# Kernel tuning notes

Measured on AMD Instinct MI355X. Metric: run time of the kernel, lower is better.

## Reference

```python
import jax, jax.numpy as jnp
import numpy as np

N_NODES = 100000
N_EDGES = 1600000
NODE_DIM = 16
EDGE_DIM = 16
OUT_DIM = 16
H = 64  # edge/node/global hidden size
N_GRAPHS = 1


def _glorot(key, shape):
    fan_in, fan_out = shape[0], shape[1]
    lim = np.sqrt(6.0 / (fan_in + fan_out))
    return jax.random.uniform(key, shape, jnp.float32, -lim, lim)


def setup_inputs() -> dict:
    key = jax.random.key(0)
    ks = jax.random.split(key, 16)
    x = jax.random.normal(ks[0], (N_NODES, NODE_DIM), jnp.float32)
    edge_attr = jax.random.normal(ks[1], (N_EDGES, EDGE_DIM), jnp.float32)
    u = jax.random.normal(ks[2], (N_GRAPHS, H), jnp.float32)
    senders = jax.random.randint(ks[3], (N_EDGES,), 0, N_NODES, jnp.int32)
    receivers = jax.random.randint(ks[4], (N_EDGES,), 0, N_NODES, jnp.int32)
    node_gidx = jnp.zeros((N_NODES,), jnp.int32)
    edge_gidx = jnp.zeros((N_EDGES,), jnp.int32)
    # EdgeBlock MLP: in = edge + 2*node + global_h
    W_eb = _glorot(ks[5], (EDGE_DIM + 2 * NODE_DIM + H, H)); b_eb = jnp.zeros((H,), jnp.float32)
    # NodeBlock MLP: in = node + edge_h + global_h
    W_nb = _glorot(ks[6], (NODE_DIM + H + H, H)); b_nb = jnp.zeros((H,), jnp.float32)
    # GlobalBlock MLP: in = node_h + edge_h + global_h
    W_gb = _glorot(ks[7], (H + H + H, H)); b_gb = jnp.zeros((H,), jnp.float32)
    # node decoder: in = 2*edge_h + node_h + global_h -> H -> out
    W_d1 = _glorot(ks[8], (2 * H + H + H, H)); b_d1 = jnp.zeros((H,), jnp.float32)
    W_d2 = _glorot(ks[9], (H, OUT_DIM)); b_d2 = jnp.zeros((OUT_DIM,), jnp.float32)
    return dict(x=x, edge_attr=edge_attr, u=u, senders=senders, receivers=receivers,
                node_gidx=node_gidx, edge_gidx=edge_gidx,
                W_eb=W_eb, b_eb=b_eb, W_nb=W_nb, b_nb=b_nb, W_gb=W_gb, b_gb=b_gb,
                W_d1=W_d1, b_d1=b_d1, W_d2=W_d2, b_d2=b_d2)


def _segment_mean(data, ids, num_segments):
    s = jax.ops.segment_sum(data, ids, num_segments=num_segments)
    cnt = jax.ops.segment_sum(jnp.ones((data.shape[0], 1), data.dtype), ids, num_segments=num_segments)
    return s / jnp.maximum(cnt, 1.0)


def reference(x, edge_attr, u, senders, receivers, node_gidx, edge_gidx,
              W_eb, b_eb, W_nb, b_nb, W_gb, b_gb, W_d1, b_d1, W_d2, b_d2):
    # ---- GN1: EdgeBlock (gather -> concat -> linear+relu) ----
    e_in = jnp.concatenate([edge_attr, x[receivers], x[senders], u[edge_gidx]], axis=-1)  # [E, 112]
    e_h = jax.nn.relu(e_in @ W_eb + b_eb)  # [E, H]
    # ---- GN1: NodeBlock (scatter_add of received edges) ----
    agg_recv = jax.ops.segment_sum(e_h, receivers, num_segments=x.shape[0])  # [N, H]
    n_in = jnp.concatenate([agg_recv, x, u[node_gidx]], axis=-1)
    n_h = jax.nn.relu(n_in @ W_nb + b_nb)  # [N, H]
    # ---- GN1: GlobalBlock (scatter_mean reductions) ----
    e_mean = _segment_mean(e_h, edge_gidx, u.shape[0])  # [B, H]
    n_mean = _segment_mean(n_h, node_gidx, u.shape[0])  # [B, H]
    g_in = jnp.concatenate([e_mean, n_mean, u], axis=-1)
    u2 = jax.nn.relu(g_in @ W_gb + b_gb)  # [B, H]
    # ---- GN2: node decoder block (scatter_mean sent + received edges) ----
    agg_recv2 = _segment_mean(e_h, receivers, x.shape[0])
    agg_sent2 = _segment_mean(e_h, senders, x.shape[0])
    d_in = jnp.concatenate([agg_recv2, agg_sent2, n_h, u2[node_gidx]], axis=-1)  # [N, 256]
    out = jax.nn.relu(d_in @ W_d1 + b_d1) @ W_d2 + b_d2  # [N, out_dim]
    return out
```

## Files before the change

kernel.cpp:

```cpp
#include <hip/hip_runtime.h>


typedef unsigned int uint;
typedef unsigned short ushort;
typedef __attribute__((ext_vector_type(8))) short bf16x8;
typedef __attribute__((ext_vector_type(4))) float f32x4;

#define BW 128
#define BSHIFT 7
#define NBMAX 784
#define DC 4096
#define EMASK 0x1FFFFFu
#define OMASK 0x1FFFFu

#define LDF4(p) (*reinterpret_cast<const float4*>(p))

__device__ __forceinline__ ushort f2bf(float f) {
  uint u = __float_as_uint(f);
  u += 0x7FFFu + ((u >> 16) & 1u);
  return (ushort)(u >> 16);
}

__device__ __forceinline__ int aswz(int row, int kb) {
  return row * 64 + ((kb ^ (row & 7)) << 3);
}
__device__ __forceinline__ int nswz(int row, int kb) {
  return row * 128 + (((kb & 8) | ((kb ^ row) & 7)) << 3);
}
__device__ __forceinline__ int aswz192(int row, int kb) {
  return row * 192 + (((kb & 24) | ((kb ^ row) & 7)) << 3);
}

__global__ __launch_bounds__(256) void init_kernel(
    const float* __restrict__ x, ushort* __restrict__ xb, int n16,
    const float* __restrict__ u, const float* __restrict__ W_eb,
    const float* __restrict__ b_eb, const float* __restrict__ W_nb,
    const float* __restrict__ b_nb, const float* __restrict__ W_d1,
    const float* __restrict__ W_d2, float* __restrict__ eb_init,
    float* __restrict__ nb_init, ushort* __restrict__ wt_lin,
    ushort* __restrict__ wnb_img, ushort* __restrict__ wtd1_img,
    ushort* __restrict__ w2_img) {
  if (blockIdx.x == 0) {
    int j = threadIdx.x;
    if (j >= 64) return;
    float ae = b_eb[j], an = b_nb[j];
    for (int k = 0; k < 64; ++k) {
      float uk = u[k];
      ae = fmaf(uk, W_eb[(48 + k) * 64 + j], ae);
      an = fmaf(uk, W_nb[(80 + k) * 64 + j], an);
    }
    eb_init[j] = ae;
    nb_init[j] = an;
    for (int k = 0; k < 64; ++k)
      wt_lin[j * 64 + k] = (k < 48) ? f2bf(W_eb[k * 64 + j]) : (ushort)0;
    for (int k = 0; k < 128; ++k) {
      ushort v = (k < 80) ? f2bf(W_nb[k * 64 + j]) : (ushort)0;
      wnb_img[nswz(j, k >> 3) + (k & 7)] = v;
    }
    for (int k = 0; k < 192; ++k)
      wtd1_img[aswz192(j, k >> 3) + (k & 7)] = f2bf(W_d1[k * 64 + j]);
    if (j < 16)
      for (int k = 0; k < 64; ++k)
        w2_img[aswz(j, k >> 3) + (k & 7)] = f2bf(W_d2[k * 16 + j]);
    return;
  }
  int i = (blockIdx.x - 1) * 256 + threadIdx.x;
  if (i * 4 >= n16) return;
  float4 a = LDF4(x + i * 4);
  ushort4 o = {f2bf(a.x), f2bf(a.y), f2bf(a.z), f2bf(a.w)};
  *reinterpret_cast<ushort4*>(xb + i * 4) = o;
}

__global__ __launch_bounds__(256) void bcount_kernel(
    const int* __restrict__ receivers, const int* __restrict__ senders,
    uint* __restrict__ bcnt_r, uint* __restrict__ bcnt_s, int E, int NB) {
  __shared__ uint hr[NBMAX], hs[NBMAX];
  int t = threadIdx.x;
  for (int i = t; i < NB; i += 256) { hr[i] = 0; hs[i] = 0; }
  __syncthreads();
  int stride = gridDim.x * 256;
  for (int e = blockIdx.x * 256 + t; e < E; e += stride) {
    atomicAdd(&hr[receivers[e] >> BSHIFT], 1u);
    atomicAdd(&hs[senders[e] >> BSHIFT], 1u);
  }
  __syncthreads();
  for (int i = t; i < NB; i += 256) {
    if (hr[i]) atomicAdd(&bcnt_r[i], hr[i]);
    if (hs[i]) atomicAdd(&bcnt_s[i], hs[i]);
  }
}

__global__ __launch_bounds__(256) void bscan_kernel(
    const uint* __restrict__ bcnt_r, const uint* __restrict__ bcnt_s,
    uint* __restrict__ start_r, uint* __restrict__ start_s,
    uint* __restrict__ cur_r, uint* __restrict__ cur_s, int E, int NB) {
  __shared__ uint ts[256];
  int t = threadIdx.x;
  #pragma unroll
  for (int pass = 0; pass < 2; ++pass) {
    const uint* cnt = pass ? bcnt_s : bcnt_r;
    uint* start = pass ? start_s : start_r;
    uint* cur = pass ? cur_s : cur_r;
    uint loc[4]; uint tsum = 0;
    #pragma unroll
    for (int q = 0; q < 4; ++q) {
      int i = t * 4 + q;
      loc[q] = (i < NB) ? cnt[i] : 0;
      tsum += loc[q];
    }
    ts[t] = tsum;
    __syncthreads();
    for (int off = 1; off < 256; off <<= 1) {
      uint a = (t >= off) ? ts[t - off] : 0;
      __syncthreads();
      ts[t] += a;
      __syncthreads();
    }
    uint run = ts[t] - tsum;
    #pragma unroll
    for (int q = 0; q < 4; ++q) {
      int i = t * 4 + q;
      if (i < NB) { start[i] = run; cur[i] = run; run += loc[q]; }
    }
    if (t == 0) start[NB] = (uint)E;
    __syncthreads();
  }
}

__global__ __launch_bounds__(256) void distribute_kernel(
    const int* __restrict__ receivers, const int* __restrict__ senders,
    uint* __restrict__ gcur_r, uint* __restrict__ gcur_s,
    uint2* __restrict__ tmp_r, uint2* __restrict__ tmp_s, int E, int NB) {
  __shared__ uint hist[NBMAX], lstart[NBMAX], cur[NBMAX], gbase[NBMAX];
  __shared__ uint2 ids[DC];
  __shared__ ushort idsB[DC];
  __shared__ uint ts[256];
  int dir = blockIdx.x & 1;
  const int* key = dir ? senders : receivers;
  const int* oth = dir ? receivers : senders;
  uint* g_cursor = dir ? gcur_s : gcur_r;
  uint2* tmp = dir ? tmp_s : tmp_r;
  int t = threadIdx.x;
  int base = (blockIdx.x >> 1) * DC;
  int cact = min(DC, E - base);
  for (int i = t; i < NB; i += 256) hist[i] = 0;
  __syncthreads();
  for (int k = 0; k < DC / 256; ++k) {
    int j = k * 256 + t;
    if (j < cact) atomicAdd(&hist[key[base + j] >> BSHIFT], 1u);
  }
  __syncthreads();
  {
    uint loc[4]; uint tsum = 0;
    #pragma unroll
    for (int q = 0; q < 4; ++q) {
      int i = t * 4 + q;
      loc[q] = (i < NB) ? hist[i] : 0;
      tsum += loc[q];
    }
    ts[t] = tsum;
    __syncthreads();
    for (int off = 1; off < 256; off <<= 1) {
      uint a = (t >= off) ? ts[t - off] : 0;
      __syncthreads();
      ts[t] += a;
      __syncthreads();
    }
    uint run = ts[t] - tsum;
    #pragma unroll
    for (int q = 0; q < 4; ++q) {
      int i = t * 4 + q;
      if (i < NB) { lstart[i] = run; cur[i] = run; run += loc[q]; }
    }
  }
  __syncthreads();
  for (int i = t; i < NB; i += 256)
    if (hist[i]) gbase[i] = atomicAdd(&g_cursor[i], hist[i]);
  for (int k = 0; k < DC / 256; ++k) {
    int j = k * 256 + t;
    if (j < cact) {
      int e = base + j;
      int kk = key[e];
      uint b = (uint)(kk >> BSHIFT);
      uint slot = atomicAdd(&cur[b], 1u);
      ids[slot] = uint2{((uint)(kk & (BW - 1)) << 21) | (uint)e,
                        (uint)oth[e]};
      idsB[slot] = (ushort)b;
    }
  }
  __syncthreads();
  for (int j = t; j < cact; j += 256) {
    uint b2 = idsB[j];
    tmp[gbase[b2] + ((uint)j - lstart[b2])] = ids[j];
  }
}

__global__ __launch_bounds__(256) void bucketsort_kernel(
    const uint2* __restrict__ tmp_r, const uint2* __restrict__ tmp_s,
    const uint* __restrict__ start_r, const uint* __restrict__ start_s,
    uint2* __restrict__ srt_r, uint2* __restrict__ srt_s,
    uint* __restrict__ cnt_r, uint* __restrict__ cnt_s, int N) {
  __shared__ uint hist[BW], pfx[BW], cur[BW];
  int d = blockIdx.x & 1;
  int b = blockIdx.x >> 1;
  const uint2* tmp = d ? tmp_s : tmp_r;
  const uint* start = d ? start_s : start_r;
  uint2* srt = d ? srt_s : srt_r;
  uint* cnt = d ? cnt_s : cnt_r;
  int t = threadIdx.x;
  if (t < BW) hist[t] = 0;
  __syncthreads();
  int beg = (int)start[b], end = (int)start[b + 1];
  for (int i = beg + t; i < end; i += 256)
    atomicAdd(&hist[tmp[i].x >> 21], 1u);
  __syncthreads();
  if (t < BW) pfx[t] = hist[t];
  __syncthreads();
  for (int off = 1; off < BW; off <<= 1) {
    uint a = 0;
    if (t < BW && t >= off) a = pfx[t - off];
    __syncthreads();
    if (t < BW) pfx[t] += a;
    __syncthreads();
  }
  if (t < BW) cur[t] = pfx[t] - hist[t];
  __syncthreads();
  uint bhi = (uint)b << 17;
  for (int i = beg + t; i < end; i += 256) {
    uint2 v = tmp[i];
    uint nl = v.x >> 21;
    uint p = beg + atomicAdd(&cur[nl], 1u);
    srt[p] = uint2{v.x, bhi | v.y};
  }
  int nbase = b * BW;
  if (t < BW && nbase + t < N) cnt[nbase + t] = hist[t];
}

__global__ __launch_bounds__(256, 4) void escatter_kernel(
    const float* __restrict__ edge_attr, const ushort* __restrict__ xb,
    const uint2* __restrict__ srt_r, const uint2* __restrict__ srt_s,
    const ushort* __restrict__ wt_lin, const float* __restrict__ eb_init,
    float* __restrict__ sum_recv, float* __restrict__ sum_sent, int E,
    int ntiles) {
  __shared__ float Clds[4][16 * 72];
  __shared__ int nodeW[4][16];
  int t = threadIdx.x;
  int wid = t >> 6, l = t & 63;
  int lrow = l & 15, lk = l >> 4;
  bf16x8 b0[4], b1[4];
  float ebi[4];
  #pragma unroll
  for (int nt = 0; nt < 4; ++nt) {
    const ushort* wr = wt_lin + (nt * 16 + lrow) * 64;
    b0[nt] = *reinterpret_cast<const bf16x8*>(wr + lk * 8);
    b1[nt] = *reinterpret_cast<const bf16x8*>(wr + 32 + lk * 8);
    ebi[nt] = eb_init[nt * 16 + lrow];
  }
  const bf16x8 zero8 = {0, 0, 0, 0, 0, 0, 0, 0};
  int dir = blockIdx.x & 1;
  const uint2* srt = dir ? srt_s : srt_r;
  float* sum = dir ? sum_sent : sum_recv;
  int gw = (blockIdx.x >> 1) * 4 + wid;
  int nw = (gridDim.x >> 1) * 4;

  uint2 vC = {0, 0}, vN = {0, 0};
  bf16x8 a0C = zero8, a1C = zero8;

  if (gw < ntiles) {
    vC = srt[min(gw * 16 + lrow, E - 1)];
    int e = (int)(vC.x & EMASK);
    int kn = (int)((vC.y >> 17) * BW + (vC.x >> 21));
    int on = (int)(vC.y & OMASK);
    int s = dir ? kn : on;
    int r = dir ? on : kn;
    if (lk < 2) {
      const float* ap = edge_attr + (size_t)e * 16 + lk * 8;
      float4 f0 = LDF4(ap), f1 = LDF4(ap + 4);
      union { ushort h[8]; bf16x8 v; } pk;
      pk.h[0] = f2bf(f0.x); pk.h[1] = f2bf(f0.y);
      pk.h[2] = f2bf(f0.z); pk.h[3] = f2bf(f0.w);
      pk.h[4] = f2bf(f1.x); pk.h[5] = f2bf(f1.y);
      pk.h[6] = f2bf(f1.z); pk.h[7] = f2bf(f1.w);
      a0C = pk.v;
      a1C = *reinterpret_cast<const bf16x8*>(xb + (size_t)s * 16 + lk * 8);
    } else {
      a0C = *reinterpret_cast<const bf16x8*>(xb + (size_t)r * 16 +
                                             (lk - 2) * 8);
      a1C = zero8;
    }
  }
  if (gw + nw < ntiles) vN = srt[min((gw + nw) * 16 + lrow, E - 1)];

  for (int tile = gw; tile < ntiles; tile += nw) {
    bool hasN = (tile + nw) < ntiles;
    bool has2 = (tile + 2 * nw) < ntiles;
    bf16x8 a0N = zero8, a1N = zero8;
    if (hasN) {
      int e = (int)(vN.x & EMASK);
      int kn = (int)((vN.y >> 17) * BW + (vN.x >> 21));
      int on = (int)(vN.y & OMASK);
      int s = dir ? kn : on;
      int r = dir ? on : kn;
      if (lk < 2) {
        const float* ap = edge_attr + (size_t)e * 16 + lk * 8;
        float4 f0 = LDF4(ap), f1 = LDF4(ap + 4);
        union { ushort h[8]; bf16x8 v; } pk;
        pk.h[0] = f2bf(f0.x); pk.h[1] = f2bf(f0.y);
        pk.h[2] = f2bf(f0.z); pk.h[3] = f2bf(f0.w);
        pk.h[4] = f2bf(f1.x); pk.h[5] = f2bf(f1.y);
        pk.h[6] = f2bf(f1.z); pk.h[7] = f2bf(f1.w);
        a0N = pk.v;
        a1N = *reinterpret_cast<const bf16x8*>(xb + (size_t)s * 16 + lk * 8);
      } else {
        a0N = *reinterpret_cast<const bf16x8*>(xb + (size_t)r * 16 +
                                               (lk - 2) * 8);
      }
    }
    uint2 v2 = {0, 0};
    if (has2) v2 = srt[min((tile + 2 * nw) * 16 + lrow, E - 1)];
    if (lk == 0)
      nodeW[wid][lrow] = (int)((vC.y >> 17) * BW + (vC.x >> 21));
    f32x4 acc[4];
    #pragma unroll
    for (int nt = 0; nt < 4; ++nt) {
      acc[nt] = f32x4{ebi[nt], ebi[nt], ebi[nt], ebi[nt]};
      acc[nt] =
          __builtin_amdgcn_mfma_f32_16x16x32_bf16(a0C, b0[nt], acc[nt], 0, 0, 0);
      acc[nt] =
          __builtin_amdgcn_mfma_f32_16x16x32_bf16(a1C, b1[nt], acc[nt], 0, 0, 0);
    }
    int m0 = (l >> 4) * 4;
    #pragma unroll
    for (int nt = 0; nt < 4; ++nt) {
      #pragma unroll
      for (int reg = 0; reg < 4; ++reg) {
        Clds[wid][(m0 + reg) * 72 + nt * 16 + lrow] =
            fmaxf(acc[nt][reg], 0.f);
      }
    }
    int vc = min(16, E - tile * 16);
    float accum = 0.f;
    int prev = nodeW[wid][0];
    for (int mm = 0; mm < vc; ++mm) {
      int nd = nodeW[wid][mm];
      float v = Clds[wid][mm * 72 + l];
      if (nd != prev) {
        atomicAdd(&sum[(size_t)prev * 64 + l], accum);
        accum = 0.f;
        prev = nd;
      }
      accum += v;
    }
    atomicAdd(&sum[(size_t)prev * 64 + l], accum);
    vC = vN; a0C = a0N; a1C = a1N; vN = v2;
  }
}

__global__ __launch_bounds__(256, 2) void node_mfma_kernel(
    const float* __restrict__ sum_recv, const ushort* __restrict__ xb,
    const ushort* __restrict__ wnb_img, const float* __restrict__ nb_init,
    ushort* __restrict__ n_h, int N) {
  __shared__ ushort Alds[64 * 128];
  __shared__ ushort Wlds[64 * 128];
  __shared__ ushort Clds[4][16 * 72];
  int t = threadIdx.x;
  int base = blockIdx.x * 64;
  {
    const uint4* src = reinterpret_cast<const uint4*>(wnb_img);
    uint4* dst = reinterpret_cast<uint4*>(Wlds);
    #pragma unroll
    for (int i = 0; i < 4; ++i) dst[t + 256 * i] = src[t + 256 * i];
  }
  {
    int m = t >> 2, part = t & 3;
    int n = base + m;
    bool val = n < N;
    if (part < 2) {
      #pragma unroll
      for (int q = 0; q < 4; ++q) {
        int c = part * 4 + q;
        union { ushort h[8]; uint4 qq; } pk;
        if (val) {
          const float* src = sum_recv + (size_t)n * 64 + c * 8;
          float4 f0 = LDF4(src), f1 = LDF4(src + 4);
          pk.h[0] = f2bf(f0.x); pk.h[1] = f2bf(f0.y);
          pk.h[2] = f2bf(f0.z); pk.h[3] = f2bf(f0.w);
          pk.h[4] = f2bf(f1.x); pk.h[5] = f2bf(f1.y);
          pk.h[6] = f2bf(f1.z); pk.h[7] = f2bf(f1.w);
        } else {
          pk.qq = uint4{0, 0, 0, 0};
        }
        *reinterpret_cast<uint4*>(&Alds[nswz(m, c)]) = pk.qq;
      }
    } else if (part == 2) {
      uint4 w0 = {0, 0, 0, 0}, w1 = {0, 0, 0, 0};
      if (val) {
        const uint4* xp = reinterpret_cast<const uint4*>(xb + (size_t)n * 16);
        w0 = xp[0]; w1 = xp[1];
      }
      *reinterpret_cast<uint4*>(&Alds[nswz(m, 8)]) = w0;
      *reinterpret_cast<uint4*>(&Alds[nswz(m, 9)]) = w1;
      *reinterpret_cast<uint4*>(&Alds[nswz(m, 10)]) = uint4{0, 0, 0, 0};
      *reinterpret_cast<uint4*>(&Alds[nswz(m, 11)]) = uint4{0, 0, 0, 0};
    } else {
      #pragma unroll
      for (int q = 0; q < 4; ++q)
        *reinterpret_cast<uint4*>(&Alds[nswz(m, 12 + q)]) = uint4{0, 0, 0, 0};
    }
  }
  __syncthreads();
  int wid = t >> 6, l = t & 63;
  int lrow = l & 15, lk = l >> 4;
  int arow = wid * 16 + lrow;
  bf16x8 afr[4];
  #pragma unroll
  for (int g = 0; g < 4; ++g)
    afr[g] = *reinterpret_cast<const bf16x8*>(&Alds[nswz(arow, g * 4 + lk)]);
  f32x4 acc[4];
  #pragma unroll
  for (int nt = 0; nt < 4; ++nt) {
    float nbi = nb_init[nt * 16 + lrow];
    acc[nt] = f32x4{nbi, nbi, nbi, nbi};
    #pragma unroll
    for (int g = 0; g < 4; ++g) {
      bf16x8 b = *reinterpret_cast<const bf16x8*>(
          &Wlds[nswz(nt * 16 + lrow, g * 4 + lk)]);
      acc[nt] =
          __builtin_amdgcn_mfma_f32_16x16x32_bf16(afr[g], b, acc[nt], 0, 0, 0);
    }
  }
  int m0 = (l >> 4) * 4;
  #pragma unroll
  for (int nt = 0; nt < 4; ++nt) {
    #pragma unroll
    for (int reg = 0; reg < 4; ++reg) {
      Clds[wid][(m0 + reg) * 72 + nt * 16 + lrow] =
          f2bf(fmaxf(acc[nt][reg], 0.f));
    }
  }
  __syncthreads();
  int sm = l >> 2, ch = l & 3;
  int gn = base + wid * 16 + sm;
  uint4 c0 = *reinterpret_cast<const uint4*>(&Clds[wid][sm * 72 + ch * 16]);
  uint4 c1 = *reinterpret_cast<const uint4*>(&Clds[wid][sm * 72 + ch * 16 + 8]);
  if (gn < N) {
    uint4* dst = reinterpret_cast<uint4*>(n_h + (size_t)gn * 64 + ch * 16);
    dst[0] = c0;
    dst[1] = c1;
  }
}

__global__ __launch_bounds__(256) void reduce_kernel(
    const float* __restrict__ sum_recv, const ushort* __restrict__ n_h,
    float* __restrict__ e_sum, float* __restrict__ n_sum, int N) {
  __shared__ float ls[128];
  if (threadIdx.x < 128) ls[threadIdx.x] = 0.f;
  __syncthreads();
  int g = threadIdx.x & 15;
  int tid = blockIdx.x * blockDim.x + threadIdx.x;
  int row0 = tid >> 4;
  int rstride = (gridDim.x * blockDim.x) >> 4;
  float pe[4] = {0, 0, 0, 0}, pn[4] = {0, 0, 0, 0};
  for (int r = row0; r < N; r += rstride) {
    float4 a = LDF4(sum_recv + (size_t)r * 64 + g * 4);
    uint2 b = *reinterpret_cast<const uint2*>(n_h + (size_t)r * 64 + g * 4);
    pe[0] += a.x; pe[1] += a.y; pe[2] += a.z; pe[3] += a.w;
    pn[0] += __uint_as_float(b.x << 16);
    pn[1] += __uint_as_float(b.x & 0xFFFF0000u);
    pn[2] += __uint_as_float(b.y << 16);
    pn[3] += __uint_as_float(b.y & 0xFFFF0000u);
  }
  #pragma unroll
  for (int i = 0; i < 4; ++i) {
    atomicAdd(&ls[g * 4 + i], pe[i]);
    atomicAdd(&ls[64 + g * 4 + i], pn[i]);
  }
  __syncthreads();
  if (threadIdx.x < 64) {
    atomicAdd(&e_sum[threadIdx.x], ls[threadIdx.x]);
    atomicAdd(&n_sum[threadIdx.x], ls[64 + threadIdx.x]);
  }
}

__global__ void global_kernel(const float* __restrict__ u,
                              const float* __restrict__ e_sum,
                              const float* __restrict__ n_sum,
                              const float* __restrict__ W_gb,
                              const float* __restrict__ b_gb,
                              const float* __restrict__ W_d1,
                              const float* __restrict__ b_d1,
                              float* __restrict__ d1_init, float Ef, float Nf) {
  __shared__ float gin[192];
  __shared__ float u2s[64];
  int j = threadIdx.x;
  gin[j] = e_sum[j] / Ef;
  gin[64 + j] = n_sum[j] / Nf;
  gin[128 + j] = u[j];
  __syncthreads();
  float a = b_gb[j];
  for (int k = 0; k < 192; ++k) a = fmaf(gin[k], W_gb[k * 64 + j], a);
  u2s[j] = fmaxf(a, 0.f);
  __syncthreads();
  float d = b_d1[j];
  for (int k = 0; k < 64; ++k) d = fmaf(u2s[k], W_d1[(192 + k) * 64 + j], d);
  d1_init[j] = d;
}

__global__ __launch_bounds__(256, 2) void decoder_mfma_kernel(
    const float* __restrict__ sum_recv, const float* __restrict__ sum_sent,
    const uint* __restrict__ cnt_r, const uint* __restrict__ cnt_s,
    const ushort* __restrict__ n_h, const ushort* __restrict__ wtd1_img,
    const float* __restrict__ d1_init, const ushort* __restrict__ w2_img,
    const float* __restrict__ b_d2, float* __restrict__ out, int N) {
  __shared__ ushort Alds[64 * 192];
  __shared__ ushort Wlds[64 * 192];
  __shared__ ushort Hlds[64 * 64];
  __shared__ ushort W2lds[16 * 64];
  int t = threadIdx.x;
  int base = blockIdx.x * 64;
  {
    const uint4* src = reinterpret_cast<const uint4*>(wtd1_img);
    uint4* dst = reinterpret_cast<uint4*>(Wlds);
    #pragma unroll
    for (int i = 0; i < 6; ++i) dst[t + 256 * i] = src[t + 256 * i];
    if (t < 128)
      reinterpret_cast<uint4*>(W2lds)[t] =
          reinterpret_cast<const uint4*>(w2_img)[t];
  }
  {
    int m = t >> 2;
    int n = base + m;
    bool val = n < N;
    float invr = 0.f, invs = 0.f;
    if (val) {
      invr = 1.f / fmaxf((float)cnt_r[n], 1.f);
      invs = 1.f / fmaxf((float)cnt_s[n], 1.f);
    }
    int c0 = (t & 3) * 6;
    for (int c = c0; c < c0 + 6; ++c) {
      union { ushort h[8]; uint4 q; } pk;
      if (val) {
        if (c >= 16) {
          pk.q = *reinterpret_cast<const uint4*>(n_h + (size_t)n * 64 +
                                                 (c - 16) * 8);
        } else {
          const float* src;
          float scl;
          if (c < 8) { src = sum_recv + (size_t)n * 64 + c * 8; scl = invr; }
          else       { src = sum_sent + (size_t)n * 64 + (c - 8) * 8; scl = invs; }
          float4 f0 = LDF4(src), f1 = LDF4(src + 4);
          pk.h[0] = f2bf(f0.x * scl); pk.h[1] = f2bf(f0.y * scl);
          pk.h[2] = f2bf(f0.z * scl); pk.h[3] = f2bf(f0.w * scl);
          pk.h[4] = f2bf(f1.x * scl); pk.h[5] = f2bf(f1.y * scl);
          pk.h[6] = f2bf(f1.z * scl); pk.h[7] = f2bf(f1.w * scl);
        }
      } else {
        pk.q = uint4{0, 0, 0, 0};
      }
      *reinterpret_cast<uint4*>(&Alds[aswz192(m, c)]) = pk.q;
    }
  }
  __syncthreads();
  int wid = t >> 6, l = t & 63;
  int lrow = l & 15, lk = l >> 4;
  int arow = wid * 16 + lrow;
  bf16x8 afr[6];
  #pragma unroll
  for (int g = 0; g < 6; ++g)
    afr[g] = *reinterpret_cast<const bf16x8*>(&Alds[aswz192(arow, g * 4 + lk)]);
  f32x4 acc[4];
  #pragma unroll
  for (int nt = 0; nt < 4; ++nt) {
    float di = d1_init[nt * 16 + lrow];
    acc[nt] = f32x4{di, di, di, di};
    #pragma unroll
    for (int g = 0; g < 6; ++g) {
      bf16x8 b = *reinterpret_cast<const bf16x8*>(
          &Wlds[aswz192(nt * 16 + lrow, g * 4 + lk)]);
      acc[nt] =
          __builtin_amdgcn_mfma_f32_16x16x32_bf16(afr[g], b, acc[nt], 0, 0, 0);
    }
  }
  int m0 = (l >> 4) * 4;
  #pragma unroll
  for (int nt = 0; nt < 4; ++nt) {
    #pragma unroll
    for (int reg = 0; reg < 4; ++reg) {
      int hm = wid * 16 + m0 + reg;
      int hn = nt * 16 + lrow;
      Hlds[hm * 64 + (((hn >> 3) ^ (hm & 7)) << 3) + (hn & 7)] =
          f2bf(fmaxf(acc[nt][reg], 0.f));
    }
  }
  __syncthreads();
  bf16x8 a20 = *reinterpret_cast<const bf16x8*>(&Hlds[aswz(arow, lk)]);
  bf16x8 a21 = *reinterpret_cast<const bf16x8*>(&Hlds[aswz(arow, 4 + lk)]);
  bf16x8 b20 = *reinterpret_cast<const bf16x8*>(&W2lds[aswz(lrow, lk)]);
  bf16x8 b21 = *reinterpret_cast<const bf16x8*>(&W2lds[aswz(lrow, 4 + lk)]);
  float bi = b_d2[lrow];
  f32x4 o = f32x4{bi, bi, bi, bi};
  o = __builtin_amdgcn_mfma_f32_16x16x32_bf16(a20, b20, o, 0, 0, 0);
  o = __builtin_amdgcn_mfma_f32_16x16x32_bf16(a21, b21, o, 0, 0, 0);
  #pragma unroll
  for (int reg = 0; reg < 4; ++reg) {
    int ge = base + wid * 16 + m0 + reg;
    if (ge < N) out[(size_t)ge * 16 + lrow] = o[reg];
  }
}

extern "C" void kernel_launch(void* const* d_in, const int* in_sizes, int n_in,
                              void* d_out, int out_size, void* d_ws,
                              size_t ws_size, hipStream_t stream) {
  const float* x         = (const float*)d_in[0];
  const float* edge_attr = (const float*)d_in[1];
  const float* u         = (const float*)d_in[2];
  const int*   senders   = (const int*)d_in[3];
  const int*   receivers = (const int*)d_in[4];
  const float* W_eb = (const float*)d_in[7];
  const float* b_eb = (const float*)d_in[8];
  const float* W_nb = (const float*)d_in[9];
  const float* b_nb = (const float*)d_in[10];
  const float* W_gb = (const float*)d_in[11];
  const float* b_gb = (const float*)d_in[12];
  const float* W_d1 = (const float*)d_in[13];
  const float* b_d1 = (const float*)d_in[14];
  const float* W_d2 = (const float*)d_in[15];
  const float* b_d2 = (const float*)d_in[16];

  int N = in_sizes[0] / 16;
  int E = in_sizes[1] / 16;
  int NB = (N + BW - 1) >> BSHIFT;
  int NDB = (E + DC - 1) / DC;
  int ntiles = (E + 15) / 16;

  char* w = (char*)d_ws;
  float* sum_recv = (float*)w;       w += (size_t)N * 64 * 4;
  float* sum_sent = (float*)w;       w += (size_t)N * 64 * 4;
  ushort* n_h = (ushort*)w;          w += (size_t)N * 64 * 2;
  uint2* tmp_r = (uint2*)w;          w += (size_t)E * 8;
  uint2* tmp_s = (uint2*)w;          w += (size_t)E * 8;
  uint2* srt_r = (uint2*)w;          w += (size_t)E * 8;
  uint2* srt_s = (uint2*)w;          w += (size_t)E * 8;
  uint* cnt_r = (uint*)w;            w += (size_t)N * 4;
  uint* cnt_s = (uint*)w;            w += (size_t)N * 4;
  ushort* xb = (ushort*)w;           w += (size_t)N * 16 * 2;
  ushort* wt_lin = (ushort*)w;       w += (size_t)64 * 64 * 2;
  ushort* wnb_img = (ushort*)w;      w += (size_t)64 * 128 * 2;
  ushort* wtd1_img = (ushort*)w;     w += (size_t)64 * 192 * 2;
  ushort* w2_img = (ushort*)w;       w += (size_t)16 * 64 * 2;
  uint* start_r = (uint*)w;          w += (size_t)(NB + 1) * 4;
  uint* start_s = (uint*)w;          w += (size_t)(NB + 1) * 4;
  uint* cur_r = (uint*)w;            w += (size_t)NB * 4;
  uint* cur_s = (uint*)w;            w += (size_t)NB * 4;
  uint* bcnt_r = (uint*)w;           w += (size_t)NBMAX * 4;
  uint* bcnt_s = (uint*)w;           w += (size_t)NBMAX * 4;
  float* e_sum = (float*)w;          w += 64 * 4;
  float* n_sum = (float*)w;          w += 64 * 4;
  float* eb_init = (float*)w;        w += 64 * 4;
  float* nb_init = (float*)w;        w += 64 * 4;
  float* d1_init = (float*)w;        w += 64 * 4;

  size_t zero_bytes = (size_t)(2 * NBMAX + 128) * 4;
  hipMemsetAsync(bcnt_r, 0, zero_bytes, stream);
  hipMemsetAsync(sum_recv, 0, (size_t)N * 128 * 4, stream);

  hipLaunchKernelGGL(init_kernel, dim3(1 + (N * 16 / 4 + 255) / 256), dim3(256),
                     0, stream, x, xb, N * 16, u, W_eb, b_eb, W_nb, b_nb, W_d1,
                     W_d2, eb_init, nb_init, wt_lin, wnb_img, wtd1_img, w2_img);
  hipLaunchKernelGGL(bcount_kernel, dim3(64), dim3(256), 0, stream, receivers,
                     senders, bcnt_r, bcnt_s, E, NB);
  hipLaunchKernelGGL(bscan_kernel, dim3(1), dim3(256), 0, stream, bcnt_r,
                     bcnt_s, start_r, start_s, cur_r, cur_s, E, NB);
  hipLaunchKernelGGL(distribute_kernel, dim3(2 * NDB), dim3(256), 0, stream,
                     receivers, senders, cur_r, cur_s, tmp_r, tmp_s, E, NB);
  hipLaunchKernelGGL(bucketsort_kernel, dim3(2 * NB), dim3(256), 0, stream,
                     tmp_r, tmp_s, start_r, start_s, srt_r, srt_s, cnt_r,
                     cnt_s, N);
  hipLaunchKernelGGL(escatter_kernel, dim3(4096), dim3(256), 0, stream,
                     edge_attr, xb, srt_r, srt_s, wt_lin, eb_init, sum_recv,
                     sum_sent, E, ntiles);
  hipLaunchKernelGGL(node_mfma_kernel, dim3((N + 63) / 64), dim3(256), 0,
                     stream, sum_recv, xb, wnb_img, nb_init, n_h, N);
  hipLaunchKernelGGL(reduce_kernel, dim3(256), dim3(256), 0, stream, sum_recv,
                     n_h, e_sum, n_sum, N);
  hipLaunchKernelGGL(global_kernel, dim3(1), dim3(64), 0, stream, u, e_sum,
                     n_sum, W_gb, b_gb, W_d1, b_d1, d1_init, (float)E,
                     (float)N);
  hipLaunchKernelGGL(decoder_mfma_kernel, dim3((N + 63) / 64), dim3(256), 0,
                     stream, sum_recv, sum_sent, cnt_r, cnt_s, n_h, wtd1_img,
                     d1_init, w2_img, b_d2, (float*)d_out, N);
}
```

Before: 416.2 us.

## Fuse bucket count into init, global reductions into node kernel, global MLP into decoder

Merges the bucket-count kernel into the init kernel as extra blocks, folds the edge and node mean reductions into node_mfma_kernel's epilogue, and recomputes the global MLP (u2 and d1_init) redundantly in every decoder block. The escatter segmented reduction now precomputes segment boundaries with a ballot instead of comparing node ids on every row. The goal is to remove three kernel launches and a separate pass over sum_recv and n_h. In exchange, each decoder block repeats a 192x64 plus 64x64 matvec on 64 threads, and every node block issues atomics to e_sum and n_sum.

```diff
diff --git a/kernel.cpp b/kernel.cpp
--- a/kernel.cpp
+++ b/kernel.cpp
@@ -32,7 +32,9 @@
 }
 
 __global__ __launch_bounds__(256) void init_kernel(
-    const float* __restrict__ x, ushort* __restrict__ xb, int n16,
+    const float* __restrict__ x, ushort* __restrict__ xb, int n16, int nxb,
+    const int* __restrict__ receivers, const int* __restrict__ senders,
+    uint* __restrict__ bcnt_r, uint* __restrict__ bcnt_s, int E, int NB,
     const float* __restrict__ u, const float* __restrict__ W_eb,
     const float* __restrict__ b_eb, const float* __restrict__ W_nb,
     const float* __restrict__ b_nb, const float* __restrict__ W_d1,
@@ -64,22 +66,21 @@
         w2_img[aswz(j, k >> 3) + (k & 7)] = f2bf(W_d2[k * 16 + j]);
     return;
   }
-  int i = (blockIdx.x - 1) * 256 + threadIdx.x;
-  if (i * 4 >= n16) return;
-  float4 a = LDF4(x + i * 4);
-  ushort4 o = {f2bf(a.x), f2bf(a.y), f2bf(a.z), f2bf(a.w)};
-  *reinterpret_cast<ushort4*>(xb + i * 4) = o;
-}
-
-__global__ __launch_bounds__(256) void bcount_kernel(
-    const int* __restrict__ receivers, const int* __restrict__ senders,
-    uint* __restrict__ bcnt_r, uint* __restrict__ bcnt_s, int E, int NB) {
+  if (blockIdx.x <= nxb) {
+    int i = (blockIdx.x - 1) * 256 + threadIdx.x;
+    if (i * 4 >= n16) return;
+    float4 a = LDF4(x + i * 4);
+    ushort4 o = {f2bf(a.x), f2bf(a.y), f2bf(a.z), f2bf(a.w)};
+    *reinterpret_cast<ushort4*>(xb + i * 4) = o;
+    return;
+  }
   __shared__ uint hr[NBMAX], hs[NBMAX];
   int t = threadIdx.x;
+  int bid = blockIdx.x - 1 - nxb;
   for (int i = t; i < NB; i += 256) { hr[i] = 0; hs[i] = 0; }
   __syncthreads();
-  int stride = gridDim.x * 256;
-  for (int e = blockIdx.x * 256 + t; e < E; e += stride) {
+  int stride = 64 * 256;
+  for (int e = bid * 256 + t; e < E; e += stride) {
     atomicAdd(&hr[receivers[e] >> BSHIFT], 1u);
     atomicAdd(&hs[senders[e] >> BSHIFT], 1u);
   }
@@ -318,8 +319,8 @@
     }
     uint2 v2 = {0, 0};
     if (has2) v2 = srt[min((tile + 2 * nw) * 16 + lrow, E - 1)];
-    if (lk == 0)
-      nodeW[wid][lrow] = (int)((vC.y >> 17) * BW + (vC.x >> 21));
+    int myNode = (int)((vC.y >> 17) * BW + (vC.x >> 21));
+    if (lk == 0) nodeW[wid][lrow] = myNode;
     f32x4 acc[4];
     #pragma unroll
     for (int nt = 0; nt < 4; ++nt) {
@@ -339,19 +340,20 @@
       }
     }
     int vc = min(16, E - tile * 16);
+    uint bmask = (uint)__ballot(lrow > 0 &&
+                                nodeW[wid][lrow] != nodeW[wid][lrow - 1]) &
+                 0xFFFFu;
     float accum = 0.f;
-    int prev = nodeW[wid][0];
+    int segstart = 0;
     for (int mm = 0; mm < vc; ++mm) {
-      int nd = nodeW[wid][mm];
-      float v = Clds[wid][mm * 72 + l];
-      if (nd != prev) {
-        atomicAdd(&sum[(size_t)prev * 64 + l], accum);
+      accum += Clds[wid][mm * 72 + l];
+      bool fin = (mm == vc - 1) || ((bmask >> (mm + 1)) & 1u);
+      if (fin) {
+        atomicAdd(&sum[(size_t)nodeW[wid][segstart] * 64 + l], accum);
         accum = 0.f;
-        prev = nd;
+        segstart = mm + 1;
       }
-      accum += v;
-    }
-    atomicAdd(&sum[(size_t)prev * 64 + l], accum);
+    }
     vC = vN; a0C = a0N; a1C = a1N; vN = v2;
   }
 }
@@ -359,7 +361,8 @@
 __global__ __launch_bounds__(256, 2) void node_mfma_kernel(
     const float* __restrict__ sum_recv, const ushort* __restrict__ xb,
     const ushort* __restrict__ wnb_img, const float* __restrict__ nb_init,
-    ushort* __restrict__ n_h, int N) {
+    ushort* __restrict__ n_h, float* __restrict__ e_sum,
+    float* __restrict__ n_sum, int N) {
   __shared__ ushort Alds[64 * 128];
   __shared__ ushort Wlds[64 * 128];
   __shared__ ushort Clds[4][16 * 72];
@@ -448,74 +451,45 @@
     dst[0] = c0;
     dst[1] = c1;
   }
-}
-
-__global__ __launch_bounds__(256) void reduce_kernel(
-    const float* __restrict__ sum_recv, const ushort* __restrict__ n_h,
-    float* __restrict__ e_sum, float* __restrict__ n_sum, int N) {
-  __shared__ float ls[128];
-  if (threadIdx.x < 128) ls[threadIdx.x] = 0.f;
-  __syncthreads();
-  int g = threadIdx.x & 15;
-  int tid = blockIdx.x * blockDim.x + threadIdx.x;
-  int row0 = tid >> 4;
-  int rstride = (gridDim.x * blockDim.x) >> 4;
-  float pe[4] = {0, 0, 0, 0}, pn[4] = {0, 0, 0, 0};
-  for (int r = row0; r < N; r += rstride) {
-    float4 a = LDF4(sum_recv + (size_t)r * 64 + g * 4);
-    uint2 b = *reinterpret_cast<const uint2*>(n_h + (size_t)r * 64 + g * 4);
-    pe[0] += a.x; pe[1] += a.y; pe[2] += a.z; pe[3] += a.w;
-    pn[0] += __uint_as_float(b.x << 16);
-    pn[1] += __uint_as_float(b.x & 0xFFFF0000u);
-    pn[2] += __uint_as_float(b.y << 16);
-    pn[3] += __uint_as_float(b.y & 0xFFFF0000u);
-  }
-  #pragma unroll
-  for (int i = 0; i < 4; ++i) {
-    atomicAdd(&ls[g * 4 + i], pe[i]);
-    atomicAdd(&ls[64 + g * 4 + i], pn[i]);
-  }
-  __syncthreads();
-  if (threadIdx.x < 64) {
-    atomicAdd(&e_sum[threadIdx.x], ls[threadIdx.x]);
-    atomicAdd(&n_sum[threadIdx.x], ls[64 + threadIdx.x]);
-  }
-}
-
-__global__ void global_kernel(const float* __restrict__ u,
-                              const float* __restrict__ e_sum,
-                              const float* __restrict__ n_sum,
-                              const float* __restrict__ W_gb,
-                              const float* __restrict__ b_gb,
-                              const float* __restrict__ W_d1,
-                              const float* __restrict__ b_d1,
-                              float* __restrict__ d1_init, float Ef, float Nf) {
-  __shared__ float gin[192];
-  __shared__ float u2s[64];
-  int j = threadIdx.x;
-  gin[j] = e_sum[j] / Ef;
-  gin[64 + j] = n_sum[j] / Nf;
-  gin[128 + j] = u[j];
-  __syncthreads();
-  float a = b_gb[j];
-  for (int k = 0; k < 192; ++k) a = fmaf(gin[k], W_gb[k * 64 + j], a);
-  u2s[j] = fmaxf(a, 0.f);
-  __syncthreads();
-  float d = b_d1[j];
-  for (int k = 0; k < 64; ++k) d = fmaf(u2s[k], W_d1[(192 + k) * 64 + j], d);
-  d1_init[j] = d;
+  float* scr = reinterpret_cast<float*>(Alds);
+  {
+    int col = t & 63, rg = t >> 6;
+    float pe = 0.f, pn = 0.f;
+    #pragma unroll
+    for (int rr = 0; rr < 16; ++rr) {
+      int n = base + rg * 16 + rr;
+      if (n < N) {
+        pe += sum_recv[(size_t)n * 64 + col];
+        pn += __uint_as_float((uint)Clds[rg][rr * 72 + col] << 16);
+      }
+    }
+    scr[rg * 64 + col] = pe;
+    scr[256 + rg * 64 + col] = pn;
+  }
+  __syncthreads();
+  if (t < 64) {
+    float se = scr[t] + scr[64 + t] + scr[128 + t] + scr[192 + t];
+    float sn = scr[256 + t] + scr[320 + t] + scr[384 + t] + scr[448 + t];
+    atomicAdd(&e_sum[t], se);
+    atomicAdd(&n_sum[t], sn);
+  }
 }
 
 __global__ __launch_bounds__(256, 2) void decoder_mfma_kernel(
     const float* __restrict__ sum_recv, const float* __restrict__ sum_sent,
     const uint* __restrict__ cnt_r, const uint* __restrict__ cnt_s,
     const ushort* __restrict__ n_h, const ushort* __restrict__ wtd1_img,
-    const float* __restrict__ d1_init, const ushort* __restrict__ w2_img,
-    const float* __restrict__ b_d2, float* __restrict__ out, int N) {
+    const ushort* __restrict__ w2_img, const float* __restrict__ b_d2,
+    const float* __restrict__ u, const float* __restrict__ e_sum,
+    const float* __restrict__ n_sum, const float* __restrict__ W_gb,
+    const float* __restrict__ b_gb, const float* __restrict__ W_d1,
+    const float* __restrict__ b_d1, float* __restrict__ out, float invE,
+    float invN, int N) {
   __shared__ ushort Alds[64 * 192];
   __shared__ ushort Wlds[64 * 192];
   __shared__ ushort Hlds[64 * 64];
   __shared__ ushort W2lds[16 * 64];
+  __shared__ float gin[192], u2s[64], d1i[64];
   int t = threadIdx.x;
   int base = blockIdx.x * 64;
   {
@@ -560,6 +534,23 @@
       *reinterpret_cast<uint4*>(&Alds[aswz192(m, c)]) = pk.q;
     }
   }
+  if (t < 64) {
+    gin[t] = e_sum[t] * invE;
+    gin[64 + t] = n_sum[t] * invN;
+    gin[128 + t] = u[t];
+  }
+  __syncthreads();
+  if (t < 64) {
+    float a = b_gb[t];
+    for (int k = 0; k < 192; ++k) a = fmaf(gin[k], W_gb[k * 64 + t], a);
+    u2s[t] = fmaxf(a, 0.f);
+  }
+  __syncthreads();
+  if (t < 64) {
+    float d = b_d1[t];
+    for (int k = 0; k < 64; ++k) d = fmaf(u2s[k], W_d1[(192 + k) * 64 + t], d);
+    d1i[t] = d;
+  }
   __syncthreads();
   int wid = t >> 6, l = t & 63;
   int lrow = l & 15, lk = l >> 4;
@@ -571,7 +562,7 @@
   f32x4 acc[4];
   #pragma unroll
   for (int nt = 0; nt < 4; ++nt) {
-    float di = d1_init[nt * 16 + lrow];
+    float di = d1i[nt * 16 + lrow];
     acc[nt] = f32x4{di, di, di, di};
     #pragma unroll
     for (int g = 0; g < 6; ++g) {
@@ -632,6 +623,7 @@
   int NB = (N + BW - 1) >> BSHIFT;
   int NDB = (E + DC - 1) / DC;
   int ntiles = (E + 15) / 16;
+  int nxb = (N * 16 / 4 + 255) / 256;
 
   char* w = (char*)d_ws;
   float* sum_recv = (float*)w;       w += (size_t)N * 64 * 4;
@@ -658,17 +650,15 @@
   float* n_sum = (float*)w;          w += 64 * 4;
   float* eb_init = (float*)w;        w += 64 * 4;
   float* nb_init = (float*)w;        w += 64 * 4;
-  float* d1_init = (float*)w;        w += 64 * 4;
 
   size_t zero_bytes = (size_t)(2 * NBMAX + 128) * 4;
   hipMemsetAsync(bcnt_r, 0, zero_bytes, stream);
   hipMemsetAsync(sum_recv, 0, (size_t)N * 128 * 4, stream);
 
-  hipLaunchKernelGGL(init_kernel, dim3(1 + (N * 16 / 4 + 255) / 256), dim3(256),
-                     0, stream, x, xb, N * 16, u, W_eb, b_eb, W_nb, b_nb, W_d1,
-                     W_d2, eb_init, nb_init, wt_lin, wnb_img, wtd1_img, w2_img);
-  hipLaunchKernelGGL(bcount_kernel, dim3(64), dim3(256), 0, stream, receivers,
-                     senders, bcnt_r, bcnt_s, E, NB);
+  hipLaunchKernelGGL(init_kernel, dim3(1 + nxb + 64), dim3(256), 0, stream, x,
+                     xb, N * 16, nxb, receivers, senders, bcnt_r, bcnt_s, E,
+                     NB, u, W_eb, b_eb, W_nb, b_nb, W_d1, W_d2, eb_init,
+                     nb_init, wt_lin, wnb_img, wtd1_img, w2_img);
   hipLaunchKernelGGL(bscan_kernel, dim3(1), dim3(256), 0, stream, bcnt_r,
                      bcnt_s, start_r, start_s, cur_r, cur_s, E, NB);
   hipLaunchKernelGGL(distribute_kernel, dim3(2 * NDB), dim3(256), 0, stream,
@@ -680,13 +670,10 @@
                      edge_attr, xb, srt_r, srt_s, wt_lin, eb_init, sum_recv,
                      sum_sent, E, ntiles);
   hipLaunchKernelGGL(node_mfma_kernel, dim3((N + 63) / 64), dim3(256), 0,
-                     stream, sum_recv, xb, wnb_img, nb_init, n_h, N);
-  hipLaunchKernelGGL(reduce_kernel, dim3(256), dim3(256), 0, stream, sum_recv,
-                     n_h, e_sum, n_sum, N);
-  hipLaunchKernelGGL(global_kernel, dim3(1), dim3(64), 0, stream, u, e_sum,
-                     n_sum, W_gb, b_gb, W_d1, b_d1, d1_init, (float)E,
-                     (float)N);
+                     stream, sum_recv, xb, wnb_img, nb_init, n_h, e_sum,
+                     n_sum, N);
   hipLaunchKernelGGL(decoder_mfma_kernel, dim3((N + 63) / 64), dim3(256), 0,
                      stream, sum_recv, sum_sent, cnt_r, cnt_s, n_h, wtd1_img,
-                     d1_init, w2_img, b_d2, (float*)d_out, N);
-}
+                     w2_img, b_d2, u, e_sum, n_sum, W_gb, b_gb, W_d1, b_d1,
+                     (float*)d_out, 1.0f / (float)E, 1.0f / (float)N, N);
+}
```

New measurement: 414.2 us. No clear change (-0.5%).
